# Kernel optimization log

Measured on AMD Instinct MI355X. Metric: run time of the kernel, lower is better.

The kernel has to match this reference:

```python
import jax, jax.numpy as jnp
import numpy as np

B = 16            # num sequences (decode: 1 query token each)
MAX_BLOCKS = 256  # blocks per sequence
BLOCK_SIZE = 16
NUM_BLOCKS = B * MAX_BLOCKS
HQ, HKV, HD = 32, 8, 128
SCALE = HD ** -0.5
NEG = -1e30


def setup_inputs() -> dict:
    key = jax.random.key(0)
    ks = jax.random.split(key, 6)
    q = jax.random.normal(ks[0], (B, HQ, HD), jnp.float32)
    k = jax.random.normal(ks[1], (B, HKV, HD), jnp.float32)
    v = jax.random.normal(ks[2], (B, HKV, HD), jnp.float32)
    k_cache = jax.random.normal(ks[3], (NUM_BLOCKS, BLOCK_SIZE, HKV, HD), jnp.float32)
    v_cache = jax.random.normal(ks[4], (NUM_BLOCKS, BLOCK_SIZE, HKV, HD), jnp.float32)
    # each sequence owns a disjoint contiguous set of blocks
    block_tables = jnp.arange(B * MAX_BLOCKS, dtype=jnp.int64).reshape(B, MAX_BLOCKS)
    seq_lens = jax.random.randint(ks[5], (B,), 2048, MAX_BLOCKS * BLOCK_SIZE + 1).astype(jnp.int64)
    last = seq_lens - 1  # slot of the token being written this step
    slot_mapping = block_tables[jnp.arange(B), last // BLOCK_SIZE] * BLOCK_SIZE + last % BLOCK_SIZE
    query_lens = jnp.ones((B,), jnp.int64)
    return {"q": q, "k": k, "v": v, "k_cache": k_cache, "v_cache": v_cache,
            "slot_mapping": slot_mapping, "block_tables": block_tables,
            "seq_lens": seq_lens, "query_lens": query_lens, "is_prefill": False}


def reference(q, k, v, k_cache, v_cache, slot_mapping, block_tables, seq_lens, query_lens, is_prefill):
    nb, bs, hkv, hd = k_cache.shape
    # write_kv_cache: scatter new k/v tokens into flat slot view of the caches
    kc = k_cache.reshape(nb * bs, hkv, hd).at[slot_mapping].set(k).reshape(nb, bs, hkv, hd)
    vc = v_cache.reshape(nb * bs, hkv, hd).at[slot_mapping].set(v).reshape(nb, bs, hkv, hd)
    b = q.shape[0]
    # gather blocks per sequence: (B, max_blocks, bs, hkv, hd) -> (B, kv_len, hkv, hd)
    K = kc[block_tables].reshape(b, -1, hkv, hd)
    V = vc[block_tables].reshape(b, -1, hkv, hd)
    kv_len = K.shape[1]
    valid = jnp.arange(kv_len)[None, :] < seq_lens[:, None]  # (B, kv_len)
    g = q.shape[1] // hkv  # GQA groups; q head k*g+j attends with kv head k
    qg = q.reshape(b, hkv, g, hd)
    scores = jnp.einsum('bkgd,bskd->bkgs', qg, K) * SCALE  # (B, hkv, g, kv_len)
    scores = jnp.where(valid[:, None, None, :], scores, NEG)
    p = jax.nn.softmax(scores, axis=-1)
    out = jnp.einsum('bkgs,bskd->bkgd', p, V).reshape(b, hkv * g, hd)
    return out
```

## Files before the change

### kernel.cpp

```cpp
#include <hip/hip_runtime.h>

#define NBATCH 16
#define MAXB 256
#define BS 16
#define HQ 32
#define HKV 8
#define G 4
#define HD 128
#define SCALE 0.08838834764831845f
#define NEGF -1.0e30f
#define NEGI -2.0e30f
#define RESCALE_THR 8.0f

__device__ __forceinline__ float dot8(const float4 a0, const float4 a1,
                                      const float4 b0, const float4 b1) {
  return a0.x*b0.x + a0.y*b0.y + a0.z*b0.z + a0.w*b0.w +
         a1.x*b1.x + a1.y*b1.y + a1.z*b1.z + a1.w*b1.w;
}

template<int CTL>
__device__ __forceinline__ float dpp_row_add(float v) {
  const int s = __builtin_amdgcn_update_dpp(0, __float_as_int(v), CTL, 0xF, 0xF, true);
  return v + __int_as_float(s);
}
__device__ __forceinline__ float row_reduce_add(float v) {
  v = dpp_row_add<0x128>(v);
  v = dpp_row_add<0x124>(v);
  v = dpp_row_add<0x122>(v);
  v = dpp_row_add<0x121>(v);
  return v;
}

__global__ __launch_bounds__(256) void pa_split(
    const float* __restrict__ q,
    const float* __restrict__ knew,
    const float* __restrict__ vnew,
    const float* __restrict__ k_cache,
    const float* __restrict__ v_cache,
    const int* __restrict__ block_tables,
    const int* __restrict__ seq_lens,
    float* __restrict__ part_ml,
    float* __restrict__ part_acc,
    int nsplit)
{
  const int hg    = blockIdx.x & 1;
  const int split = (blockIdx.x >> 1) % nsplit;
  const int b     = blockIdx.x / (2 * nsplit);
  const int h     = hg * 4 + (threadIdx.x >> 6);
  const int lane  = threadIdx.x & 63;
  const int tg    = lane >> 4;
  const int tl    = lane & 15;

  const int seq_len = seq_lens[b];
  int per = (seq_len + nsplit - 1) / nsplit;
  per = (per + 15) & ~15;
  const int s0 = split * per;
  const int s1 = min(seq_len, s0 + per);
  const int last = seq_len - 1;
  const size_t pidx = (size_t)(b*HKV + h)*nsplit + split;

  if (s0 >= seq_len) {
    if (tg == 0) {
      if (tl == 0) {
#pragma unroll
        for (int j = 0; j < G; ++j) {
          part_ml[(pidx*G + j)*2 + 0] = NEGF;
          part_ml[(pidx*G + j)*2 + 1] = 0.f;
        }
      }
      const float4 z = make_float4(0.f,0.f,0.f,0.f);
#pragma unroll
      for (int j = 0; j < G; ++j) {
        float4* ap = (float4*)(part_acc + (pidx*G + j)*HD + tl*8);
        ap[0] = z; ap[1] = z;
      }
    }
    return;
  }

  float4 q0[G], q1[G];
#pragma unroll
  for (int j = 0; j < G; ++j) {
    const float* qp = q + (size_t)(b*HQ + h*G + j)*HD + tl*8;
    q0[j] = ((const float4*)qp)[0];
    q1[j] = ((const float4*)qp)[1];
  }

  float m[G], l[G];
  float4 a0[G], a1[G];
#pragma unroll
  for (int j = 0; j < G; ++j) {
    m[j] = NEGF; l[j] = 0.f;
    a0[j] = make_float4(0.f,0.f,0.f,0.f);
    a1[j] = make_float4(0.f,0.f,0.f,0.f);
  }

  const float* knp = knew + (size_t)(b*HKV + h)*HD + tl*8;
  const float* vnp = vnew + (size_t)(b*HKV + h)*HD + tl*8;

  for (int c = s0; c < s1; c += 16) {
    const int blk = block_tables[b*MAXB + (c >> 4)];
    const size_t pbase = (size_t)blk*BS*(HKV*HD) + (size_t)h*HD + tl*8;

    float4 kr[4][2], vr[4][2];
#pragma unroll
    for (int i = 0; i < 4; ++i) {
      const int s = c + i*4 + tg;
      const float* kp = k_cache + pbase + (size_t)(i*4 + tg)*(HKV*HD);
      const float* vp = v_cache + pbase + (size_t)(i*4 + tg)*(HKV*HD);
      if (s == last) { kp = knp; vp = vnp; }
      kr[i][0] = ((const float4*)kp)[0];
      kr[i][1] = ((const float4*)kp)[1];
      vr[i][0] = ((const float4*)vp)[0];
      vr[i][1] = ((const float4*)vp)[1];
    }

#pragma unroll
    for (int i = 0; i < 4; ++i) {
      const int s = c + i*4 + tg;
      const bool valid = s < s1;
      float sc[G];
#pragma unroll
      for (int j = 0; j < G; ++j) {
        float p = dot8(q0[j], q1[j], kr[i][0], kr[i][1]);
        p = row_reduce_add(p);
        sc[j] = valid ? p * SCALE : NEGI;
      }
      bool need = false;
#pragma unroll
      for (int j = 0; j < G; ++j) need = need || (sc[j] > m[j] + RESCALE_THR);
      if (__any(need)) {
#pragma unroll
        for (int j = 0; j < G; ++j) {
          const float mn = fmaxf(m[j], sc[j]);
          const float f  = __expf(m[j] - mn);
          l[j] *= f;
          a0[j].x *= f; a0[j].y *= f; a0[j].z *= f; a0[j].w *= f;
          a1[j].x *= f; a1[j].y *= f; a1[j].z *= f; a1[j].w *= f;
          m[j] = mn;
        }
      }
#pragma unroll
      for (int j = 0; j < G; ++j) {
        const float pp = __expf(sc[j] - m[j]);
        l[j] += pp;
        a0[j].x += pp*vr[i][0].x;
        a0[j].y += pp*vr[i][0].y;
        a0[j].z += pp*vr[i][0].z;
        a0[j].w += pp*vr[i][0].w;
        a1[j].x += pp*vr[i][1].x;
        a1[j].y += pp*vr[i][1].y;
        a1[j].z += pp*vr[i][1].z;
        a1[j].w += pp*vr[i][1].w;
      }
    }
  }

#pragma unroll
  for (int mask = 16; mask <= 32; mask <<= 1) {
#pragma unroll
    for (int j = 0; j < G; ++j) {
      const float mo = __shfl_xor(m[j], mask, 64);
      const float lo = __shfl_xor(l[j], mask, 64);
      const float mn = fmaxf(m[j], mo);
      const float f0 = __expf(m[j] - mn);
      const float f1 = __expf(mo  - mn);
      l[j] = l[j]*f0 + lo*f1;
      float t;
      t = __shfl_xor(a0[j].x, mask, 64); a0[j].x = a0[j].x*f0 + t*f1;
      t = __shfl_xor(a0[j].y, mask, 64); a0[j].y = a0[j].y*f0 + t*f1;
      t = __shfl_xor(a0[j].z, mask, 64); a0[j].z = a0[j].z*f0 + t*f1;
      t = __shfl_xor(a0[j].w, mask, 64); a0[j].w = a0[j].w*f0 + t*f1;
      t = __shfl_xor(a1[j].x, mask, 64); a1[j].x = a1[j].x*f0 + t*f1;
      t = __shfl_xor(a1[j].y, mask, 64); a1[j].y = a1[j].y*f0 + t*f1;
      t = __shfl_xor(a1[j].z, mask, 64); a1[j].z = a1[j].z*f0 + t*f1;
      t = __shfl_xor(a1[j].w, mask, 64); a1[j].w = a1[j].w*f0 + t*f1;
      m[j] = mn;
    }
  }

  if (tg == 0) {
    if (tl == 0) {
#pragma unroll
      for (int j = 0; j < G; ++j) {
        part_ml[(pidx*G + j)*2 + 0] = m[j];
        part_ml[(pidx*G + j)*2 + 1] = l[j];
      }
    }
#pragma unroll
    for (int j = 0; j < G; ++j) {
      float4* ap = (float4*)(part_acc + (pidx*G + j)*HD + tl*8);
      ap[0] = a0[j];
      ap[1] = a1[j];
    }
  }
}

__global__ __launch_bounds__(128) void pa_reduce(
    const float* __restrict__ part_ml,
    const float* __restrict__ part_acc,
    float* __restrict__ out,
    int P)
{
  const int qh = blockIdx.x % HQ;
  const int b  = blockIdx.x / HQ;
  const int h  = qh >> 2;
  const int j  = qh & 3;
  const int d  = threadIdx.x;

  const size_t base = (size_t)(b*HKV + h) * P;
  float mg = NEGF;
  for (int p = 0; p < P; ++p)
    mg = fmaxf(mg, part_ml[((base + p)*G + j)*2 + 0]);

  float lsum = 0.f, asum = 0.f;
  for (int p = 0; p < P; ++p) {
    const float mm = part_ml[((base + p)*G + j)*2 + 0];
    const float ll = part_ml[((base + p)*G + j)*2 + 1];
    const float f  = __expf(mm - mg);
    lsum += f * ll;
    asum += f * part_acc[((base + p)*G + j)*HD + d];
  }
  out[(size_t)(b*HQ + qh)*HD + d] = asum / lsum;
}

extern "C" void kernel_launch(void* const* d_in, const int* in_sizes, int n_in,
                              void* d_out, int out_size, void* d_ws, size_t ws_size,
                              hipStream_t stream) {
  const float* q  = (const float*)d_in[0];
  const float* k  = (const float*)d_in[1];
  const float* v  = (const float*)d_in[2];
  const float* kc = (const float*)d_in[3];
  const float* vc = (const float*)d_in[4];
  const int* bt = (const int*)d_in[6];
  const int* sl = (const int*)d_in[7];

  int nsplit = 64;
  for (;;) {
    const size_t need = (size_t)NBATCH * HKV * nsplit * G * (2 + HD) * sizeof(float);
    if (need <= ws_size || nsplit == 1) break;
    nsplit >>= 1;
  }
  float* part_ml  = (float*)d_ws;
  float* part_acc = part_ml + (size_t)NBATCH * HKV * nsplit * G * 2;

  hipLaunchKernelGGL(pa_split, dim3(NBATCH * nsplit * 2), dim3(256), 0, stream,
                     q, k, v, kc, vc, bt, sl, part_ml, part_acc, nsplit);
  hipLaunchKernelGGL(pa_reduce, dim3(NBATCH * HQ), dim3(128), 0, stream,
                     part_ml, part_acc, (float*)d_out, nsplit);
}
```

Measured before the change: 117.0 us.

## Double-buffer KV page loads and halve split count

The split kernel's page loop is restructured into a ping-pong software pipeline. The next page's K/V registers and its block table entry are loaded while the current page is being computed, so global memory latency is hidden behind the math. The number of sequence splits also drops from 64 to 32, which doubles the work per block and shrinks the reduce pass. The cost is roughly twice the K/V register footprint, which may lower occupancy, and fewer blocks in flight.

```diff
diff --git a/kernel.cpp b/kernel.cpp
--- a/kernel.cpp
+++ b/kernel.cpp
@@ -97,12 +97,11 @@
 
   const float* knp = knew + (size_t)(b*HKV + h)*HD + tl*8;
   const float* vnp = vnew + (size_t)(b*HKV + h)*HD + tl*8;
-
-  for (int c = s0; c < s1; c += 16) {
-    const int blk = block_tables[b*MAXB + (c >> 4)];
+  const int btbase = b * MAXB;
+
+  auto load_page = [&](float4 (&kr)[4][2], float4 (&vr)[4][2],
+                       const int blk, const int c) {
     const size_t pbase = (size_t)blk*BS*(HKV*HD) + (size_t)h*HD + tl*8;
-
-    float4 kr[4][2], vr[4][2];
 #pragma unroll
     for (int i = 0; i < 4; ++i) {
       const int s = c + i*4 + tg;
@@ -114,7 +113,10 @@
       vr[i][0] = ((const float4*)vp)[0];
       vr[i][1] = ((const float4*)vp)[1];
     }
-
+  };
+
+  auto compute_page = [&](const float4 (&kr)[4][2], const float4 (&vr)[4][2],
+                          const int c) {
 #pragma unroll
     for (int i = 0; i < 4; ++i) {
       const int s = c + i*4 + tg;
@@ -154,6 +156,30 @@
         a1[j].w += pp*vr[i][1].w;
       }
     }
+  };
+
+  float4 ka[4][2], va[4][2], kb[4][2], vb[4][2];
+  int c = s0;
+  int blkNext = block_tables[btbase + (c >> 4)];
+  load_page(ka, va, blkNext, c);
+  if (c + 16 < s1) blkNext = block_tables[btbase + ((c + 16) >> 4)];
+
+  for (;;) {
+    if (c + 16 < s1) {
+      load_page(kb, vb, blkNext, c + 16);
+      if (c + 32 < s1) blkNext = block_tables[btbase + ((c + 32) >> 4)];
+    }
+    compute_page(ka, va, c);
+    c += 16;
+    if (c >= s1) break;
+
+    if (c + 16 < s1) {
+      load_page(ka, va, blkNext, c + 16);
+      if (c + 32 < s1) blkNext = block_tables[btbase + ((c + 32) >> 4)];
+    }
+    compute_page(kb, vb, c);
+    c += 16;
+    if (c >= s1) break;
   }
 
 #pragma unroll
@@ -235,7 +261,7 @@
   const int* bt = (const int*)d_in[6];
   const int* sl = (const int*)d_in[7];
 
-  int nsplit = 64;
+  int nsplit = 32;
   for (;;) {
     const size_t need = (size_t)NBATCH * HKV * nsplit * G * (2 + HD) * sizeof(float);
     if (need <= ws_size || nsplit == 1) break;
```

Result: faster. 106.1 us (-9.3%).

## Stage paged KV through LDS with async global_load_lds double buffering

Applied to the files above, without the earlier changes.

Each block now handles all 8 KV heads of one sequence split with 512 threads, and stages 4 tokens of K and V at a time into double-buffered shared memory using global_load_lds. Compute on the current buffer overlaps the load of the next. The per-lane dimension mapping changes to interleaved float4 halves so LDS reads are contiguous. The aim is to hide memory latency and issue wide, coalesced loads, at the cost of 64KB LDS per block (lower occupancy) and a __syncthreads for every 4 tokens.

```diff
diff --git a/kernel.cpp b/kernel.cpp
--- a/kernel.cpp
+++ b/kernel.cpp
@@ -12,6 +12,10 @@
 #define NEGI -2.0e30f
 #define RESCALE_THR 8.0f
 
+typedef const __attribute__((address_space(1))) unsigned int* gas_t;
+typedef __attribute__((address_space(3))) unsigned int* las_t;
+#define GLDS(g, l) __builtin_amdgcn_global_load_lds((gas_t)(g), (las_t)(l), 16, 0, 0)
+
 __device__ __forceinline__ float dot8(const float4 a0, const float4 a1,
                                       const float4 b0, const float4 b1) {
   return a0.x*b0.x + a0.y*b0.y + a0.z*b0.z + a0.w*b0.w +
@@ -31,7 +35,7 @@
   return v;
 }
 
-__global__ __launch_bounds__(256) void pa_split(
+__global__ __launch_bounds__(512) void pa_split(
     const float* __restrict__ q,
     const float* __restrict__ knew,
     const float* __restrict__ vnew,
@@ -43,10 +47,11 @@
     float* __restrict__ part_acc,
     int nsplit)
 {
-  const int hg    = blockIdx.x & 1;
-  const int split = (blockIdx.x >> 1) % nsplit;
-  const int b     = blockIdx.x / (2 * nsplit);
-  const int h     = hg * 4 + (threadIdx.x >> 6);
+  __shared__ float lds[2][8192];
+
+  const int b     = blockIdx.x % NBATCH;
+  const int split = blockIdx.x / NBATCH;
+  const int wv    = threadIdx.x >> 6;
   const int lane  = threadIdx.x & 63;
   const int tg    = lane >> 4;
   const int tl    = lane & 15;
@@ -57,7 +62,7 @@
   const int s0 = split * per;
   const int s1 = min(seq_len, s0 + per);
   const int last = seq_len - 1;
-  const size_t pidx = (size_t)(b*HKV + h)*nsplit + split;
+  const size_t pidx = (size_t)(b*HKV + wv)*nsplit + split;
 
   if (s0 >= seq_len) {
     if (tg == 0) {
@@ -71,8 +76,8 @@
       const float4 z = make_float4(0.f,0.f,0.f,0.f);
 #pragma unroll
       for (int j = 0; j < G; ++j) {
-        float4* ap = (float4*)(part_acc + (pidx*G + j)*HD + tl*8);
-        ap[0] = z; ap[1] = z;
+        *(float4*)(part_acc + (pidx*G + j)*HD + tl*4)      = z;
+        *(float4*)(part_acc + (pidx*G + j)*HD + 64 + tl*4) = z;
       }
     }
     return;
@@ -81,9 +86,9 @@
   float4 q0[G], q1[G];
 #pragma unroll
   for (int j = 0; j < G; ++j) {
-    const float* qp = q + (size_t)(b*HQ + h*G + j)*HD + tl*8;
-    q0[j] = ((const float4*)qp)[0];
-    q1[j] = ((const float4*)qp)[1];
+    const float* qp = q + (size_t)(b*HQ + wv*G + j)*HD;
+    q0[j] = *(const float4*)(qp + tl*4);
+    q1[j] = *(const float4*)(qp + 64 + tl*4);
   }
 
   float m[G], l[G];
@@ -95,65 +100,80 @@
     a1[j] = make_float4(0.f,0.f,0.f,0.f);
   }
 
-  const float* knp = knew + (size_t)(b*HKV + h)*HD + tl*8;
-  const float* vnp = vnew + (size_t)(b*HKV + h)*HD + tl*8;
-
-  for (int c = s0; c < s1; c += 16) {
-    const int blk = block_tables[b*MAXB + (c >> 4)];
-    const size_t pbase = (size_t)blk*BS*(HKV*HD) + (size_t)h*HD + tl*8;
-
-    float4 kr[4][2], vr[4][2];
-#pragma unroll
-    for (int i = 0; i < 4; ++i) {
-      const int s = c + i*4 + tg;
-      const float* kp = k_cache + pbase + (size_t)(i*4 + tg)*(HKV*HD);
-      const float* vp = v_cache + pbase + (size_t)(i*4 + tg)*(HKV*HD);
-      if (s == last) { kp = knp; vp = vnp; }
-      kr[i][0] = ((const float4*)kp)[0];
-      kr[i][1] = ((const float4*)kp)[1];
-      vr[i][0] = ((const float4*)vp)[0];
-      vr[i][1] = ((const float4*)vp)[1];
-    }
-
-#pragma unroll
-    for (int i = 0; i < 4; ++i) {
-      const int s = c + i*4 + tg;
-      const bool valid = s < s1;
-      float sc[G];
+  const char* kcb = (const char*)k_cache;
+  const char* vcb = (const char*)v_cache;
+  const char* knb = (const char*)knew;
+  const char* vnb = (const char*)vnew;
+  const int btbase = b * MAXB;
+
+  auto stage = [&](float* buf, const int p0) {
+    const int blk = block_tables[btbase + (p0 >> 4)];
+    const size_t pagebyte = ((size_t)blk*BS + (p0 & 15)) * (HKV*HD*4);
+    char* dst = (char*)buf;
+#pragma unroll
+    for (int j = 0; j < 2; ++j) {
+      const int off = j*8192 + wv*1024 + lane*16;
+      const char* srcK = kcb + pagebyte + off;
+      const char* srcV = vcb + pagebyte + off;
+      if (p0 + (off >> 12) == last) {
+        const int head = (off >> 9) & 7;
+        const size_t noff = (size_t)(b*HKV + head)*512 + (off & 511);
+        srcK = knb + noff;
+        srcV = vnb + noff;
+      }
+      GLDS(srcK, dst + j*8192 + wv*1024);
+      GLDS(srcV, dst + 16384 + j*8192 + wv*1024);
+    }
+  };
+
+  auto compute = [&](const float* buf, const int p0) {
+    const int sv = p0 + tg;
+    const bool valid = sv < s1;
+    const float* Kb = buf + tg*1024 + wv*128;
+    const float* Vb = Kb + 4096;
+    const float4 k0 = *(const float4*)(Kb + tl*4);
+    const float4 k1 = *(const float4*)(Kb + 64 + tl*4);
+    const float4 v0 = *(const float4*)(Vb + tl*4);
+    const float4 v1 = *(const float4*)(Vb + 64 + tl*4);
+
+    float sc[G];
+#pragma unroll
+    for (int j = 0; j < G; ++j) {
+      float p = dot8(q0[j], q1[j], k0, k1);
+      p = row_reduce_add(p);
+      sc[j] = valid ? p * SCALE : NEGI;
+    }
+    bool need = false;
+#pragma unroll
+    for (int j = 0; j < G; ++j) need = need || (sc[j] > m[j] + RESCALE_THR);
+    if (__any(need)) {
 #pragma unroll
       for (int j = 0; j < G; ++j) {
-        float p = dot8(q0[j], q1[j], kr[i][0], kr[i][1]);
-        p = row_reduce_add(p);
-        sc[j] = valid ? p * SCALE : NEGI;
-      }
-      bool need = false;
-#pragma unroll
-      for (int j = 0; j < G; ++j) need = need || (sc[j] > m[j] + RESCALE_THR);
-      if (__any(need)) {
-#pragma unroll
-        for (int j = 0; j < G; ++j) {
-          const float mn = fmaxf(m[j], sc[j]);
-          const float f  = __expf(m[j] - mn);
-          l[j] *= f;
-          a0[j].x *= f; a0[j].y *= f; a0[j].z *= f; a0[j].w *= f;
-          a1[j].x *= f; a1[j].y *= f; a1[j].z *= f; a1[j].w *= f;
-          m[j] = mn;
-        }
-      }
-#pragma unroll
-      for (int j = 0; j < G; ++j) {
-        const float pp = __expf(sc[j] - m[j]);
-        l[j] += pp;
-        a0[j].x += pp*vr[i][0].x;
-        a0[j].y += pp*vr[i][0].y;
-        a0[j].z += pp*vr[i][0].z;
-        a0[j].w += pp*vr[i][0].w;
-        a1[j].x += pp*vr[i][1].x;
-        a1[j].y += pp*vr[i][1].y;
-        a1[j].z += pp*vr[i][1].z;
-        a1[j].w += pp*vr[i][1].w;
-      }
-    }
+        const float mn = fmaxf(m[j], sc[j]);
+        const float f  = __expf(m[j] - mn);
+        l[j] *= f;
+        a0[j].x *= f; a0[j].y *= f; a0[j].z *= f; a0[j].w *= f;
+        a1[j].x *= f; a1[j].y *= f; a1[j].z *= f; a1[j].w *= f;
+        m[j] = mn;
+      }
+    }
+#pragma unroll
+    for (int j = 0; j < G; ++j) {
+      const float pp = __expf(sc[j] - m[j]);
+      l[j] += pp;
+      a0[j].x += pp*v0.x; a0[j].y += pp*v0.y; a0[j].z += pp*v0.z; a0[j].w += pp*v0.w;
+      a1[j].x += pp*v1.x; a1[j].y += pp*v1.y; a1[j].z += pp*v1.z; a1[j].w += pp*v1.w;
+    }
+  };
+
+  stage(lds[0], s0);
+  __syncthreads();
+  int cur = 0;
+  for (int p0 = s0; p0 < s1; p0 += 4) {
+    if (p0 + 4 < s1) stage(lds[cur ^ 1], p0 + 4);
+    compute(lds[cur], p0);
+    __syncthreads();
+    cur ^= 1;
   }
 
 #pragma unroll
@@ -189,9 +209,8 @@
     }
 #pragma unroll
     for (int j = 0; j < G; ++j) {
-      float4* ap = (float4*)(part_acc + (pidx*G + j)*HD + tl*8);
-      ap[0] = a0[j];
-      ap[1] = a1[j];
+      *(float4*)(part_acc + (pidx*G + j)*HD + tl*4)      = a0[j];
+      *(float4*)(part_acc + (pidx*G + j)*HD + 64 + tl*4) = a1[j];
     }
   }
 }
@@ -244,7 +263,7 @@
   float* part_ml  = (float*)d_ws;
   float* part_acc = part_ml + (size_t)NBATCH * HKV * nsplit * G * 2;
 
-  hipLaunchKernelGGL(pa_split, dim3(NBATCH * nsplit * 2), dim3(256), 0, stream,
+  hipLaunchKernelGGL(pa_split, dim3(NBATCH * nsplit), dim3(512), 0, stream,
                      q, k, v, kc, vc, bt, sl, part_ml, part_acc, nsplit);
   hipLaunchKernelGGL(pa_reduce, dim3(NBATCH * HQ), dim3(128), 0, stream,
                      part_ml, part_acc, (float*)d_out, nsplit);
```

Result: slower. 151.7 us (+29.6%).

## Software-pipeline KV page loads, reorder grid by split, halve split count

Applied to the files above, without the earlier changes.

The per-page load-then-compute loop becomes a rotating register pipeline: each 4-token group is computed, then its registers are refilled with the next page's data, and block-table lookups are prefetched two pages ahead. The grid index now maps batch fastest and split slowest, so concurrently scheduled workgroups span different sequences. The split count drops from 64 to 32, giving each workgroup more pages to amortise the pipeline and a smaller partial buffer for the reduce. The trade-offs are fewer workgroups for latency hiding and higher register pressure from holding extra in-flight loads.

```diff
diff --git a/kernel.cpp b/kernel.cpp
--- a/kernel.cpp
+++ b/kernel.cpp
@@ -44,8 +44,8 @@
     int nsplit)
 {
   const int hg    = blockIdx.x & 1;
-  const int split = (blockIdx.x >> 1) % nsplit;
-  const int b     = blockIdx.x / (2 * nsplit);
+  const int b     = (blockIdx.x >> 1) % NBATCH;
+  const int split = blockIdx.x / (2 * NBATCH);
   const int h     = hg * 4 + (threadIdx.x >> 6);
   const int lane  = threadIdx.x & 63;
   const int tg    = lane >> 4;
@@ -97,63 +97,86 @@
 
   const float* knp = knew + (size_t)(b*HKV + h)*HD + tl*8;
   const float* vnp = vnew + (size_t)(b*HKV + h)*HD + tl*8;
-
-  for (int c = s0; c < s1; c += 16) {
-    const int blk = block_tables[b*MAXB + (c >> 4)];
-    const size_t pbase = (size_t)blk*BS*(HKV*HD) + (size_t)h*HD + tl*8;
-
-    float4 kr[4][2], vr[4][2];
-#pragma unroll
-    for (int i = 0; i < 4; ++i) {
-      const int s = c + i*4 + tg;
-      const float* kp = k_cache + pbase + (size_t)(i*4 + tg)*(HKV*HD);
-      const float* vp = v_cache + pbase + (size_t)(i*4 + tg)*(HKV*HD);
-      if (s == last) { kp = knp; vp = vnp; }
-      kr[i][0] = ((const float4*)kp)[0];
-      kr[i][1] = ((const float4*)kp)[1];
-      vr[i][0] = ((const float4*)vp)[0];
-      vr[i][1] = ((const float4*)vp)[1];
-    }
-
-#pragma unroll
-    for (int i = 0; i < 4; ++i) {
-      const int s = c + i*4 + tg;
-      const bool valid = s < s1;
-      float sc[G];
+  const int btbase = b * MAXB;
+
+  auto loadG = [&](float4 (&kr)[2], float4 (&vr)[2], const int blk, const int pos) {
+    const int s = pos + tg;
+    const size_t off = ((size_t)blk*BS + (s & 15))*(HKV*HD) + (size_t)h*HD + tl*8;
+    const float* kp = k_cache + off;
+    const float* vp = v_cache + off;
+    if (s == last) { kp = knp; vp = vnp; }
+    kr[0] = ((const float4*)kp)[0];
+    kr[1] = ((const float4*)kp)[1];
+    vr[0] = ((const float4*)vp)[0];
+    vr[1] = ((const float4*)vp)[1];
+  };
+
+  auto computeG = [&](const float4 (&kr)[2], const float4 (&vr)[2], const int pos) {
+    const bool valid = (pos + tg) < s1;
+    float sc[G];
+#pragma unroll
+    for (int j = 0; j < G; ++j) {
+      float p = dot8(q0[j], q1[j], kr[0], kr[1]);
+      p = row_reduce_add(p);
+      sc[j] = valid ? p * SCALE : NEGI;
+    }
+    bool need = false;
+#pragma unroll
+    for (int j = 0; j < G; ++j) need = need || (sc[j] > m[j] + RESCALE_THR);
+    if (__any(need)) {
 #pragma unroll
       for (int j = 0; j < G; ++j) {
-        float p = dot8(q0[j], q1[j], kr[i][0], kr[i][1]);
-        p = row_reduce_add(p);
-        sc[j] = valid ? p * SCALE : NEGI;
-      }
-      bool need = false;
-#pragma unroll
-      for (int j = 0; j < G; ++j) need = need || (sc[j] > m[j] + RESCALE_THR);
-      if (__any(need)) {
-#pragma unroll
-        for (int j = 0; j < G; ++j) {
-          const float mn = fmaxf(m[j], sc[j]);
-          const float f  = __expf(m[j] - mn);
-          l[j] *= f;
-          a0[j].x *= f; a0[j].y *= f; a0[j].z *= f; a0[j].w *= f;
-          a1[j].x *= f; a1[j].y *= f; a1[j].z *= f; a1[j].w *= f;
-          m[j] = mn;
-        }
-      }
-#pragma unroll
-      for (int j = 0; j < G; ++j) {
-        const float pp = __expf(sc[j] - m[j]);
-        l[j] += pp;
-        a0[j].x += pp*vr[i][0].x;
-        a0[j].y += pp*vr[i][0].y;
-        a0[j].z += pp*vr[i][0].z;
-        a0[j].w += pp*vr[i][0].w;
-        a1[j].x += pp*vr[i][1].x;
-        a1[j].y += pp*vr[i][1].y;
-        a1[j].z += pp*vr[i][1].z;
-        a1[j].w += pp*vr[i][1].w;
-      }
-    }
+        const float mn = fmaxf(m[j], sc[j]);
+        const float f  = __expf(m[j] - mn);
+        l[j] *= f;
+        a0[j].x *= f; a0[j].y *= f; a0[j].z *= f; a0[j].w *= f;
+        a1[j].x *= f; a1[j].y *= f; a1[j].z *= f; a1[j].w *= f;
+        m[j] = mn;
+      }
+    }
+#pragma unroll
+    for (int j = 0; j < G; ++j) {
+      const float pp = __expf(sc[j] - m[j]);
+      l[j] += pp;
+      a0[j].x += pp*vr[0].x; a0[j].y += pp*vr[0].y;
+      a0[j].z += pp*vr[0].z; a0[j].w += pp*vr[0].w;
+      a1[j].x += pp*vr[1].x; a1[j].y += pp*vr[1].y;
+      a1[j].z += pp*vr[1].z; a1[j].w += pp*vr[1].w;
+    }
+  };
+
+  const int npos   = s1 - s0;
+  const int npages = (npos + 15) >> 4;
+  const int pg0    = s0 >> 4;
+
+  float4 kA[2], vA[2], kB[2], vB[2], kC[2], vC[2], kD[2], vD[2];
+
+  int blkCur  = block_tables[btbase + pg0];
+  int blkNext = block_tables[btbase + pg0 + ((npages > 1) ? 1 : 0)];
+
+  loadG(kA, vA, blkCur, s0);
+  loadG(kB, vB, blkCur, s0 + 4);
+  loadG(kC, vC, blkCur, s0 + 8);
+  loadG(kD, vD, blkCur, s0 + 12);
+
+  for (int p = 0; p < npages; ++p) {
+    const int base  = s0 + p*16;
+    const bool more = (p + 1 < npages);
+    const int blkL  = blkNext;
+    const int lbase = base + 16;
+    const int pnn   = (p + 2 < npages) ? (p + 2) : (npages - 1);
+    const int blkNN = block_tables[btbase + pg0 + pnn];
+
+    computeG(kA, vA, base);
+    if (more) loadG(kA, vA, blkL, lbase);
+    computeG(kB, vB, base + 4);
+    if (more) loadG(kB, vB, blkL, lbase + 4);
+    computeG(kC, vC, base + 8);
+    if (more) loadG(kC, vC, blkL, lbase + 8);
+    computeG(kD, vD, base + 12);
+    if (more) loadG(kD, vD, blkL, lbase + 12);
+
+    blkNext = blkNN;
   }
 
 #pragma unroll
@@ -235,7 +258,7 @@
   const int* bt = (const int*)d_in[6];
   const int* sl = (const int*)d_in[7];
 
-  int nsplit = 64;
+  int nsplit = 32;
   for (;;) {
     const size_t need = (size_t)NBATCH * HKV * nsplit * G * (2 + HD) * sizeof(float);
     if (need <= ws_size || nsplit == 1) break;
```

Measured after the change: 105.5 us. 1.11x faster.
